# Kernel optimization log

Hardware: AMD Instinct MI355X
Metric: run time of the kernel (lower is better)

Reference implementation:

```python
import jax, jax.numpy as jnp
import numpy as np

# Model config (matches init_kwargs)
B, I, H, C = 2048, 1024, 2048, 1000   # batch, input_dim, hidden_dim, num_classes
S = 8                                  # num_wavefunctions
TOPK = 256
PARTIAL_NORM = 1.0
SM_STEPS = 2                           # self_modulation_steps
EPS = 1e-8


def setup_inputs() -> dict:
    key = jax.random.key(0)
    ks = jax.random.split(key, 9)
    x      = jax.random.normal(ks[0], (B, I), jnp.float32)
    # stacked per-wavefunction Linear(input_dim, 2*hidden_dim)
    W      = jax.random.normal(ks[1], (S, 2 * H, I), jnp.float32) * (1.0 / np.sqrt(I))
    b      = jax.random.normal(ks[2], (S, 2 * H), jnp.float32) * 0.01
    phases = jax.random.normal(ks[3], (S, H), jnp.float32) * 0.1   # phase_per_dim=True
    gate_W = jax.random.normal(ks[4], (H, H), jnp.float32) * (1.0 / np.sqrt(H))
    gate_b = jax.random.normal(ks[5], (H,), jnp.float32) * 0.01
    clf_W  = jax.random.normal(ks[6], (C, H), jnp.float32) * (1.0 / np.sqrt(H))
    clf_b  = jax.random.normal(ks[7], (C,), jnp.float32) * 0.01
    return {"x": x, "W": W, "b": b, "phases": phases,
            "gate_W": gate_W, "gate_b": gate_b, "clf_W": clf_W, "clf_b": clf_b}


def reference(x, W, b, phases, gate_W, gate_b, clf_W, clf_b):
    # All wavefunction branches batched into one GEMM: [B,S,2H]
    out = jnp.einsum('bi,shi->bsh', x, W) + b[None]
    out = jnp.exp(-(out * out))                      # ArcBell activation
    alpha, beta = out[..., :H], out[..., H:]         # [B,S,H] each
    norm_sq = jnp.sum(alpha * alpha + beta * beta, axis=-1, keepdims=True) + EPS
    factor = jnp.sqrt((PARTIAL_NORM * PARTIAL_NORM) / norm_sq)  # [B,S,1]
    alpha = alpha * factor
    beta = beta * factor
    cphi = jnp.cos(phases)[None]                     # [1,S,H]
    sphi = jnp.sin(phases)[None]
    # phase rotation + complex accumulate over wavefunctions
    sup_real = jnp.sum(alpha * cphi - beta * sphi, axis=1)   # [B,H]
    sup_imag = jnp.sum(alpha * sphi + beta * cphi, axis=1)
    # self-modulation (fixed small step count -> Python loop is fine)
    for _ in range(SM_STEPS):
        mag = jnp.sqrt(sup_real * sup_real + sup_imag * sup_imag)
        gate = jax.nn.sigmoid(mag @ gate_W.T + gate_b)
        sup_real = sup_real * gate
        sup_imag = sup_imag * gate
    mag_sq = sup_real * sup_real + sup_imag * sup_imag       # [B,H]
    # top-k masked probability aggregation
    _, idx = jax.lax.top_k(mag_sq, TOPK)                     # idx: [B,TOPK]
    mask = jnp.zeros_like(mag_sq).at[jnp.arange(B)[:, None], idx].set(1.0)
    masked = mag_sq * mask
    probs = masked / (jnp.sum(masked, axis=-1, keepdims=True) + EPS)
    logits = probs @ clf_W.T + clf_b                         # [B,C]
    return logits
```

## Files before the change

### kernel.cpp

```cpp
#include <hip/hip_runtime.h>

typedef _Float16 f16;
typedef _Float16 f16x8 __attribute__((ext_vector_type(8)));
typedef _Float16 f16x4 __attribute__((ext_vector_type(4)));
typedef float f32x4 __attribute__((ext_vector_type(4)));

#define B_    2048
#define I_    1024
#define H_    2048
#define C_    1000
#define S_    8
#define N1    32768
#define TOPK_ 256

__device__ __forceinline__ void gload16(const void* g, void* l) {
  __builtin_amdgcn_global_load_lds((const __attribute__((address_space(1))) void*)g,
                                   (__attribute__((address_space(3))) void*)l,
                                   16, 0, 0);
}

#define NW8  (S_ * 2 * H_ * I_ / 8)
#define NX8  (B_ * I_ / 8)
#define NG8  (H_ * H_ / 8)
#define NC8  (1024 * H_ / 8)
#define NPH  (S_ * H_)
#define NTOT (NW8 + NX8 + NG8 + NC8 + NPH)

__global__ void prep_kernel(const float* __restrict__ W, const float* __restrict__ x,
                            const float* __restrict__ gW, const float* __restrict__ cW,
                            const float* __restrict__ ph,
                            f16* __restrict__ Wf, f16* __restrict__ xf,
                            f16* __restrict__ gWf, f16* __restrict__ cWf,
                            float* __restrict__ cphi, float* __restrict__ sphi)
{
  int i = blockIdx.x * blockDim.x + threadIdx.x;
  if (i >= NTOT) return;
  if (i < NW8 + NX8 + NG8 + NC8) {
    const float* src;
    f16* dst;
    int j = i;
    bool pad = false;
    if (j < NW8)                { src = W;  dst = Wf; }
    else if ((j -= NW8) < NX8)  { src = x;  dst = xf; }
    else if ((j -= NX8) < NG8)  { src = gW; dst = gWf; }
    else {
      j -= NG8; src = cW; dst = cWf;
      pad = (j >= C_ * H_ / 8);
    }
    f16x8 o;
    if (!pad) {
      const float4 a = reinterpret_cast<const float4*>(src)[2 * j];
      const float4 b = reinterpret_cast<const float4*>(src)[2 * j + 1];
      o = (f16x8){ (f16)a.x, (f16)a.y, (f16)a.z, (f16)a.w,
                   (f16)b.x, (f16)b.y, (f16)b.z, (f16)b.w };
    } else {
      o = (f16x8){ (f16)0.f, (f16)0.f, (f16)0.f, (f16)0.f,
                   (f16)0.f, (f16)0.f, (f16)0.f, (f16)0.f };
    }
    reinterpret_cast<f16x8*>(dst)[j] = o;
  } else {
    int j = i - (NW8 + NX8 + NG8 + NC8);
    float p = ph[j];
    cphi[j] = cosf(p);
    sphi[j] = sinf(p);
  }
}

__global__ __launch_bounds__(512, 1)
void gemm1_r4(const f16* __restrict__ A, const f16* __restrict__ Bm,
              const float* __restrict__ bias, f16* __restrict__ act)
{
  __shared__ char SL[131072];
  const int tid = threadIdx.x, lane = tid & 63, wid = tid >> 6;
  const int wr = wid >> 2, wc = wid & 3;
  const int fr = lane & 15, fq = lane >> 4;
  const int bid = blockIdx.x;
  const int swz = (bid & 7) * 128 + (bid >> 3);
  const int mt = swz & 7, nt = swz >> 3;
  const long brow = (long)mt * 256, bcol = (long)nt * 256;

  const int schunk = ((tid & 3) ^ ((tid >> 3) & 3)) * 8;
  const f16* srcP[4];
  srcP[0] = A  + (brow + (tid >> 2)) * (long)I_ + schunk;
  srcP[1] = A  + (brow + 128 + (tid >> 2)) * (long)I_ + schunk;
  srcP[2] = Bm + (bcol + (tid >> 2)) * (long)I_ + schunk;
  srcP[3] = Bm + (bcol + 128 + (tid >> 2)) * (long)I_ + schunk;

  const int co = (fq ^ ((fr >> 1) & 3)) * 16;
  const int rdA0 = (wr * 128 + fr) * 64 + co;
  const int rdB0 = 16384 + (wc * 64 + fr) * 64 + co;

  f32x4 acc[8][4] = {};

#define STG1(a, tt)                                                    \
  gload16(srcP[a] + (size_t)(tt) * 32,                                 \
          SL + ((tt) & 3) * 32768 + ((a) * 512 + tid) * 16)

  STG1(0,0); STG1(1,0); STG1(2,0); STG1(3,0);
  STG1(0,1); STG1(1,1); STG1(2,1); STG1(3,1);
  STG1(0,2); STG1(1,2); STG1(2,2); STG1(3,2);
  asm volatile("s_waitcnt vmcnt(8)" ::: "memory");
  __builtin_amdgcn_s_barrier();

#pragma unroll 1
  for (int t = 0; t < 32; ++t) {
    const char* rb = SL + (t & 3) * 32768;
    if (t < 29) { STG1(0, t + 3); STG1(1, t + 3); STG1(2, t + 3); STG1(3, t + 3); }

    f16x8 bf[4], af[8];
#pragma unroll
    for (int n = 0; n < 4; ++n) bf[n] = *(const f16x8*)(rb + rdB0 + n * 1024);
#pragma unroll
    for (int i = 0; i < 8; ++i) af[i] = *(const f16x8*)(rb + rdA0 + i * 1024);

    __builtin_amdgcn_s_setprio(1);
#pragma unroll
    for (int i = 0; i < 8; ++i)
#pragma unroll
      for (int n = 0; n < 4; ++n)
        acc[i][n] = __builtin_amdgcn_mfma_f32_16x16x32_f16(af[i], bf[n], acc[i][n], 0, 0, 0);
    __builtin_amdgcn_s_setprio(0);

    if (t < 29)       asm volatile("s_waitcnt vmcnt(8)" ::: "memory");
    else if (t == 29) asm volatile("s_waitcnt vmcnt(4)" ::: "memory");
    else              asm volatile("s_waitcnt vmcnt(0)" ::: "memory");
    __builtin_amdgcn_s_barrier();
  }
#undef STG1

  float bv[4];
#pragma unroll
  for (int n = 0; n < 4; ++n) bv[n] = bias[bcol + wc * 64 + n * 16 + fr];
#pragma unroll
  for (int m = 0; m < 8; ++m) {
    const long r0 = brow + wr * 128 + m * 16 + fq * 4;
#pragma unroll
    for (int n = 0; n < 4; ++n) {
      const long c = bcol + wc * 64 + n * 16 + fr;
#pragma unroll
      for (int j = 0; j < 4; ++j) {
        const float tt = acc[m][n][j] + bv[n];
        act[(r0 + j) * (long)N1 + c] = (f16)__expf(-tt * tt);
      }
    }
  }
}

template<int BM, int BN, int WM, int WN, int THREADS, int MINW, int EPI>
__global__ __launch_bounds__(THREADS, MINW)
void gemm_ring(const f16* __restrict__ A, const f16* __restrict__ Bmat,
               const int K, const int MT, const int ldc, const int nreal,
               const float* __restrict__ bias,
               const float* __restrict__ magin,
               float* __restrict__ mago32, f16* __restrict__ mago16,
               float* __restrict__ msqout, float* __restrict__ logits)
{
  constexpr int MREP  = BM / (WM * 16);
  constexpr int NREP  = BN / (WN * 16);
  constexpr int CA    = (BM * 64) / (THREADS * 16);
  constexpr int CB    = (BN * 64) / (THREADS * 16);
  constexpr int CALLS = CA + CB;
  constexpr int SLOT  = (BM + BN) * 32;
  __shared__ f16 SL[4 * SLOT];

  const int tid  = threadIdx.x;
  const int lane = tid & 63, wid = tid >> 6;
  const int wr = wid / WN, wc = wid % WN;
  const int fr = lane & 15, fq = lane >> 4;

  const int nwg = gridDim.x;
  const int chunk = nwg >> 3;
  const int swz = (blockIdx.x & 7) * chunk + (blockIdx.x >> 3);
  const int mt = swz % MT, nt = swz / MT;
  const long brow = (long)mt * BM, bcol = (long)nt * BN;

  const f16* srcA[CA];
  const f16* srcB[CB];
#pragma unroll
  for (int a = 0; a < CA; ++a) {
    const int r = (a * THREADS + tid) >> 2;
    const int cs = (tid & 3) ^ ((r >> 1) & 3);
    srcA[a] = A + (size_t)(brow + r) * K + cs * 8;
  }
#pragma unroll
  for (int a = 0; a < CB; ++a) {
    const int r = (a * THREADS + tid) >> 2;
    const int cs = (tid & 3) ^ ((r >> 1) & 3);
    srcB[a] = Bmat + (size_t)(bcol + r) * K + cs * 8;
  }

  int ard[MREP], brd[NREP];
#pragma unroll
  for (int m = 0; m < MREP; ++m) {
    const int r = wr * MREP * 16 + m * 16 + fr;
    ard[m] = r * 32 + ((fq ^ ((r >> 1) & 3)) * 8);
  }
#pragma unroll
  for (int n = 0; n < NREP; ++n) {
    const int r = wc * NREP * 16 + n * 16 + fr;
    brd[n] = r * 32 + ((fq ^ ((r >> 1) & 3)) * 8);
  }

  f32x4 acc[MREP][NREP] = {};
  const int ntile = K >> 5;

#define STAGE_TILE(tt)                                                         \
  do {                                                                         \
    f16* D = &SL[((tt) & 3) * SLOT];                                           \
    const long kt = (long)(tt) * 32;                                           \
    _Pragma("unroll")                                                          \
    for (int a = 0; a < CA; ++a)                                               \
      gload16(srcA[a] + kt, D + a * THREADS * 8 + wid * 512);                  \
    _Pragma("unroll")                                                          \
    for (int a = 0; a < CB; ++a)                                               \
      gload16(srcB[a] + kt, D + BM * 32 + a * THREADS * 8 + wid * 512);        \
  } while (0)

  STAGE_TILE(0); STAGE_TILE(1); STAGE_TILE(2);

  for (int t = 0; t < ntile; ++t) {
    if (t + 3 < ntile) STAGE_TILE(t + 3);
    if (t < ntile - 3)       asm volatile("s_waitcnt vmcnt(%0)" :: "i"(3 * CALLS) : "memory");
    else if (t == ntile - 3) asm volatile("s_waitcnt vmcnt(%0)" :: "i"(2 * CALLS) : "memory");
    else if (t == ntile - 2) asm volatile("s_waitcnt vmcnt(%0)" :: "i"(1 * CALLS) : "memory");
    else                     asm volatile("s_waitcnt vmcnt(0)" ::: "memory");
    __builtin_amdgcn_s_barrier();
    asm volatile("" ::: "memory");

    const f16* SA = &SL[(t & 3) * SLOT];
    const f16* SB = SA + BM * 32;
    f16x8 af[MREP], bf[NREP];
#pragma unroll
    for (int m = 0; m < MREP; ++m) af[m] = *(const f16x8*)(SA + ard[m]);
#pragma unroll
    for (int n = 0; n < NREP; ++n) bf[n] = *(const f16x8*)(SB + brd[n]);

    __builtin_amdgcn_s_setprio(1);
#pragma unroll
    for (int m = 0; m < MREP; ++m)
#pragma unroll
      for (int n = 0; n < NREP; ++n)
        acc[m][n] = __builtin_amdgcn_mfma_f32_16x16x32_f16(af[m], bf[n], acc[m][n], 0, 0, 0);
    __builtin_amdgcn_s_setprio(0);
    asm volatile("" ::: "memory");
    __builtin_amdgcn_s_barrier();
  }
#undef STAGE_TILE

#pragma unroll
  for (int m = 0; m < MREP; ++m) {
    const long r0 = brow + wr * MREP * 16 + m * 16 + fq * 4;
#pragma unroll
    for (int n = 0; n < NREP; ++n) {
      const long c = bcol + wc * NREP * 16 + n * 16 + fr;
      float bv;
      if (EPI == 2) bv = (c < nreal) ? bias[c] : 0.f;
      else          bv = bias[c];
#pragma unroll
      for (int j = 0; j < 4; ++j) {
        const long r = r0 + j;
        const float t = acc[m][n][j] + bv;
        if (EPI == 1) {
          const float g = 1.f / (1.f + __expf(-t));
          const long idx = r * (long)ldc + c;
          const float v = magin[idx] * g;
          if (msqout) msqout[idx] = v * v;
          else { mago32[idx] = v; mago16[idx] = (f16)v; }
        } else {
          if (c < nreal) logits[r * (long)nreal + c] = t;
        }
      }
    }
  }
}

__global__ __launch_bounds__(512)
void normsup_kernel(const f16* __restrict__ act,
                    const float* __restrict__ cphi, const float* __restrict__ sphi,
                    float* __restrict__ mag32, f16* __restrict__ mag16)
{
  __shared__ float buf[4096];
  __shared__ float red[8];
  const int b = blockIdx.x, tid = threadIdx.x;
  const int lane = tid & 63, wv = tid >> 6;
  float sr[4] = {0, 0, 0, 0}, si[4] = {0, 0, 0, 0};
  const f16* base = act + (size_t)b * N1;

  for (int s = 0; s < S_; ++s) {
    f16x8 v = *(const f16x8*)(base + s * 4096 + tid * 8);
    float ls = 0.f;
#pragma unroll
    for (int e = 0; e < 8; ++e) {
      float f = (float)v[e];
      buf[tid * 8 + e] = f;
      ls += f * f;
    }
#pragma unroll
    for (int o = 32; o > 0; o >>= 1) ls += __shfl_down(ls, o);
    if (lane == 0) red[wv] = ls;
    __syncthreads();
    const float tot = red[0] + red[1] + red[2] + red[3] + red[4] + red[5] + red[6] + red[7];
    const float factor = 1.f / sqrtf(tot + 1e-8f);

    const float4 c4 = *(const float4*)(cphi + s * H_ + tid * 4);
    const float4 s4 = *(const float4*)(sphi + s * H_ + tid * 4);
    const float4 a4 = *(const float4*)(&buf[tid * 4]);
    const float4 b4 = *(const float4*)(&buf[2048 + tid * 4]);
    sr[0] += factor * (a4.x * c4.x - b4.x * s4.x); si[0] += factor * (a4.x * s4.x + b4.x * c4.x);
    sr[1] += factor * (a4.y * c4.y - b4.y * s4.y); si[1] += factor * (a4.y * s4.y + b4.y * c4.y);
    sr[2] += factor * (a4.z * c4.z - b4.z * s4.z); si[2] += factor * (a4.z * s4.z + b4.z * c4.z);
    sr[3] += factor * (a4.w * c4.w - b4.w * s4.w); si[3] += factor * (a4.w * s4.w + b4.w * c4.w);
    __syncthreads();
  }

  const size_t o = (size_t)b * H_ + tid * 4;
  const float m0 = sqrtf(sr[0] * sr[0] + si[0] * si[0]);
  const float m1 = sqrtf(sr[1] * sr[1] + si[1] * si[1]);
  const float m2 = sqrtf(sr[2] * sr[2] + si[2] * si[2]);
  const float m3 = sqrtf(sr[3] * sr[3] + si[3] * si[3]);
  *(float4*)(mag32 + o) = make_float4(m0, m1, m2, m3);
  f16x4 mh = { (f16)m0, (f16)m1, (f16)m2, (f16)m3 };
  *(f16x4*)(mag16 + o) = mh;
}

__global__ __launch_bounds__(256)
void topk_kernel(const float* __restrict__ msq, f16* __restrict__ probs)
{
  __shared__ unsigned vals[2048];
  __shared__ int hist[256];
  __shared__ int scn[256];
  __shared__ int sdig, sknew;
  __shared__ float wsum[4];
  const int b = blockIdx.x, tid = threadIdx.x;
  const unsigned* row = (const unsigned*)(msq + (size_t)b * H_);

  uint4 v0 = *(const uint4*)(row + tid * 8);
  uint4 v1 = *(const uint4*)(row + tid * 8 + 4);
  vals[tid * 8 + 0] = v0.x; vals[tid * 8 + 1] = v0.y;
  vals[tid * 8 + 2] = v0.z; vals[tid * 8 + 3] = v0.w;
  vals[tid * 8 + 4] = v1.x; vals[tid * 8 + 5] = v1.y;
  vals[tid * 8 + 6] = v1.z; vals[tid * 8 + 7] = v1.w;
  __syncthreads();

  int k = TOPK_;
  unsigned prefix = 0, pmask = 0;
  for (int pass = 0; pass < 4; ++pass) {
    const int sh = 24 - pass * 8;
    hist[tid] = 0;
    __syncthreads();
#pragma unroll
    for (int e = 0; e < 8; ++e) {
      unsigned v = vals[tid * 8 + e];
      if ((v & pmask) == prefix) atomicAdd(&hist[(v >> sh) & 255u], 1);
    }
    __syncthreads();
    const int own = hist[tid];
    int sc = own;
    scn[tid] = sc;
    __syncthreads();
    for (int o2 = 1; o2 < 256; o2 <<= 1) {
      int add = (tid + o2 < 256) ? scn[tid + o2] : 0;
      __syncthreads();
      sc += add; scn[tid] = sc;
      __syncthreads();
    }
    if (sc >= k && (sc - own) < k) { sdig = tid; sknew = k - (sc - own); }
    __syncthreads();
    prefix |= ((unsigned)sdig) << sh;
    pmask  |= 0xFFu << sh;
    k = sknew;
    __syncthreads();
  }

  const unsigned T = prefix;
  const int krem = k;
  unsigned vl[8];
  int eqc = 0;
#pragma unroll
  for (int e = 0; e < 8; ++e) { vl[e] = vals[tid * 8 + e]; if (vl[e] == T) eqc++; }
  int sc2 = eqc;
  scn[tid] = sc2;
  __syncthreads();
  for (int o2 = 1; o2 < 256; o2 <<= 1) {
    int add = (tid >= o2) ? scn[tid - o2] : 0;
    __syncthreads();
    sc2 += add; scn[tid] = sc2;
    __syncthreads();
  }
  int rank = sc2 - eqc;
  float ls = 0.f;
  bool sel[8];
#pragma unroll
  for (int e = 0; e < 8; ++e) {
    const unsigned v = vl[e];
    bool s_ = false;
    if (v > T) s_ = true;
    else if (v == T) { s_ = (rank < krem); ++rank; }
    sel[e] = s_;
    if (s_) ls += __uint_as_float(v);
  }
#pragma unroll
  for (int o2 = 32; o2 > 0; o2 >>= 1) ls += __shfl_down(ls, o2);
  if ((tid & 63) == 0) wsum[tid >> 6] = ls;
  __syncthreads();
  const float tot = wsum[0] + wsum[1] + wsum[2] + wsum[3];
  const float inv = 1.f / (tot + 1e-8f);
  f16x8 ov;
#pragma unroll
  for (int e = 0; e < 8; ++e)
    ov[e] = sel[e] ? (f16)(__uint_as_float(vl[e]) * inv) : (f16)0.f;
  *(f16x8*)(probs + (size_t)b * H_ + tid * 8) = ov;
}

extern "C" void kernel_launch(void* const* d_in, const int* in_sizes, int n_in,
                              void* d_out, int out_size, void* d_ws, size_t ws_size,
                              hipStream_t stream)
{
  const float* x  = (const float*)d_in[0];
  const float* W  = (const float*)d_in[1];
  const float* bb = (const float*)d_in[2];
  const float* ph = (const float*)d_in[3];
  const float* gW = (const float*)d_in[4];
  const float* gb = (const float*)d_in[5];
  const float* cW = (const float*)d_in[6];
  const float* cb = (const float*)d_in[7];
  float* out = (float*)d_out;

  char* base = (char*)d_ws;
  size_t off = 0;
  auto take = [&](size_t bytes) -> char* {
    char* r = base + off;
    off += (bytes + 255) & ~(size_t)255;
    return r;
  };
  f16*   Wf    = (f16*)  take((size_t)S_ * 2 * H_ * I_ * 2);
  f16*   xf    = (f16*)  take((size_t)B_ * I_ * 2);
  f16*   gWf   = (f16*)  take((size_t)H_ * H_ * 2);
  f16*   cWf   = (f16*)  take((size_t)1024 * H_ * 2);
  float* cphi  = (float*)take((size_t)S_ * H_ * 4);
  float* sphi  = (float*)take((size_t)S_ * H_ * 4);
  f16*   act   = (f16*)  take((size_t)B_ * N1 * 2);
  float* mag0f = (float*)take((size_t)B_ * H_ * 4);
  f16*   mag0h = (f16*)  take((size_t)B_ * H_ * 2);
  float* mag1f = (float*)take((size_t)B_ * H_ * 4);
  f16*   mag1h = (f16*)  take((size_t)B_ * H_ * 2);
  float* msq   = (float*)take((size_t)B_ * H_ * 4);
  f16*   probs = (f16*)  take((size_t)B_ * H_ * 2);
  (void)ws_size; (void)in_sizes; (void)n_in; (void)out_size;

  prep_kernel<<<(NTOT + 255) / 256, 256, 0, stream>>>(
      W, x, gW, cW, ph, Wf, xf, gWf, cWf, cphi, sphi);

  gemm1_r4<<<(B_ / 256) * (N1 / 256), 512, 0, stream>>>(xf, Wf, bb, act);

  normsup_kernel<<<B_, 512, 0, stream>>>(act, cphi, sphi, mag0f, mag0h);

  gemm_ring<128, 128, 2, 2, 256, 2, 1><<<(B_ / 128) * (H_ / 128), 256, 0, stream>>>(
      mag0h, gWf, H_, B_ / 128, H_, H_, gb,
      mag0f, mag1f, mag1h, nullptr, nullptr);

  gemm_ring<128, 128, 2, 2, 256, 2, 1><<<(B_ / 128) * (H_ / 128), 256, 0, stream>>>(
      mag1h, gWf, H_, B_ / 128, H_, H_, gb,
      mag1f, nullptr, nullptr, msq, nullptr);

  topk_kernel<<<B_, 256, 0, stream>>>(msq, probs);

  gemm_ring<128, 64, 2, 2, 256, 3, 2><<<(B_ / 128) * (1024 / 64), 256, 0, stream>>>(
      probs, cWf, H_, B_ / 128, 0, C_, cb,
      nullptr, nullptr, nullptr, nullptr, out);
}
```

Before: 374.5 us.

## Convert fp32 W to fp16 inside GEMM1 and retile gate GEMMs

Result: slower. 430.4 us (+14.9%).

```diff
diff --git a/kernel.cpp b/kernel.cpp
--- a/kernel.cpp
+++ b/kernel.cpp
@@ -19,29 +19,27 @@
                                    16, 0, 0);
 }
 
-#define NW8  (S_ * 2 * H_ * I_ / 8)
 #define NX8  (B_ * I_ / 8)
 #define NG8  (H_ * H_ / 8)
 #define NC8  (1024 * H_ / 8)
 #define NPH  (S_ * H_)
-#define NTOT (NW8 + NX8 + NG8 + NC8 + NPH)
-
-__global__ void prep_kernel(const float* __restrict__ W, const float* __restrict__ x,
+#define NTOT (NX8 + NG8 + NC8 + NPH)
+
+__global__ void prep_kernel(const float* __restrict__ x,
                             const float* __restrict__ gW, const float* __restrict__ cW,
                             const float* __restrict__ ph,
-                            f16* __restrict__ Wf, f16* __restrict__ xf,
+                            f16* __restrict__ xf,
                             f16* __restrict__ gWf, f16* __restrict__ cWf,
                             float* __restrict__ cphi, float* __restrict__ sphi)
 {
   int i = blockIdx.x * blockDim.x + threadIdx.x;
   if (i >= NTOT) return;
-  if (i < NW8 + NX8 + NG8 + NC8) {
+  if (i < NX8 + NG8 + NC8) {
     const float* src;
     f16* dst;
     int j = i;
     bool pad = false;
-    if (j < NW8)                { src = W;  dst = Wf; }
-    else if ((j -= NW8) < NX8)  { src = x;  dst = xf; }
+    if (j < NX8)                { src = x;  dst = xf; }
     else if ((j -= NX8) < NG8)  { src = gW; dst = gWf; }
     else {
       j -= NG8; src = cW; dst = cWf;
@@ -59,7 +57,7 @@
     }
     reinterpret_cast<f16x8*>(dst)[j] = o;
   } else {
-    int j = i - (NW8 + NX8 + NG8 + NC8);
+    int j = i - (NX8 + NG8 + NC8);
     float p = ph[j];
     cphi[j] = cosf(p);
     sphi[j] = sinf(p);
@@ -67,10 +65,10 @@
 }
 
 __global__ __launch_bounds__(512, 1)
-void gemm1_r4(const f16* __restrict__ A, const f16* __restrict__ Bm,
-              const float* __restrict__ bias, f16* __restrict__ act)
-{
-  __shared__ char SL[131072];
+void gemm1_w32(const f16* __restrict__ A, const float* __restrict__ BW,
+               const float* __restrict__ bias, f16* __restrict__ act)
+{
+  __shared__ char SL[98304];
   const int tid = threadIdx.x, lane = tid & 63, wid = tid >> 6;
   const int wr = wid >> 2, wc = wid & 3;
   const int fr = lane & 15, fq = lane >> 4;
@@ -80,38 +78,62 @@
   const long brow = (long)mt * 256, bcol = (long)nt * 256;
 
   const int schunk = ((tid & 3) ^ ((tid >> 3) & 3)) * 8;
-  const f16* srcP[4];
-  srcP[0] = A  + (brow + (tid >> 2)) * (long)I_ + schunk;
-  srcP[1] = A  + (brow + 128 + (tid >> 2)) * (long)I_ + schunk;
-  srcP[2] = Bm + (bcol + (tid >> 2)) * (long)I_ + schunk;
-  srcP[3] = Bm + (bcol + 128 + (tid >> 2)) * (long)I_ + schunk;
+  const f16* srcA0 = A + (brow + (tid >> 2)) * (long)I_ + schunk;
+  const f16* srcA1 = A + (brow + 128 + (tid >> 2)) * (long)I_ + schunk;
+
+  const int rB   = tid >> 1;
+  const int aSel = (tid & 1) ^ ((tid >> 3) & 1);
+  const int beta = (tid >> 2) & 1;
+  const float* bsrc = BW + (size_t)(bcol + rB) * I_ + aSel * 16;
+  char* wbase = SL + 65536 + tid * 32;
 
   const int co = (fq ^ ((fr >> 1) & 3)) * 16;
   const int rdA0 = (wr * 128 + fr) * 64 + co;
-  const int rdB0 = 16384 + (wc * 64 + fr) * 64 + co;
+  const int rdB0 = (wc * 64 + fr) * 64 + co;
 
   f32x4 acc[8][4] = {};
 
-#define STG1(a, tt)                                                    \
-  gload16(srcP[a] + (size_t)(tt) * 32,                                 \
-          SL + ((tt) & 3) * 32768 + ((a) * 512 + tid) * 16)
-
-  STG1(0,0); STG1(1,0); STG1(2,0); STG1(3,0);
-  STG1(0,1); STG1(1,1); STG1(2,1); STG1(3,1);
-  STG1(0,2); STG1(1,2); STG1(2,2); STG1(3,2);
-  asm volatile("s_waitcnt vmcnt(8)" ::: "memory");
-  __builtin_amdgcn_s_barrier();
+#define STGA(a, tt)                                                     \
+  gload16(((a) ? srcA1 : srcA0) + (size_t)(tt) * 32,                    \
+          SL + ((tt) & 3) * 16384 + ((a) * 512 + tid) * 16)
+#define LOADB(tt, v0, v1, v2, v3)                                       \
+  do { const float4* bp = (const float4*)(bsrc + (size_t)(tt) * 32);    \
+       v0 = bp[0]; v1 = bp[1]; v2 = bp[2]; v3 = bp[3]; } while (0)
+#define WRITEB(slot, v0, v1, v2, v3)                                    \
+  do { f16x8 h0 = { (f16)v0.x, (f16)v0.y, (f16)v0.z, (f16)v0.w,         \
+                    (f16)v1.x, (f16)v1.y, (f16)v1.z, (f16)v1.w };       \
+       f16x8 h1 = { (f16)v2.x, (f16)v2.y, (f16)v2.z, (f16)v2.w,         \
+                    (f16)v3.x, (f16)v3.y, (f16)v3.z, (f16)v3.w };       \
+       char* wb = wbase + (slot) * 16384;                               \
+       *(f16x8*)(wb + beta * 16) = h0;                                  \
+       *(f16x8*)(wb + (beta ^ 1) * 16) = h1; } while (0)
+
+  {
+    float4 p0, p1, p2, p3;
+    LOADB(0, p0, p1, p2, p3);
+    asm volatile("" ::: "memory");
+    STGA(0,0); STGA(1,0); STGA(0,1); STGA(1,1); STGA(0,2); STGA(1,2);
+    asm volatile("s_waitcnt vmcnt(4)" ::: "memory");
+    WRITEB(0, p0, p1, p2, p3);
+    asm volatile("s_waitcnt lgkmcnt(0)" ::: "memory");
+    __builtin_amdgcn_s_barrier();
+  }
 
 #pragma unroll 1
   for (int t = 0; t < 32; ++t) {
-    const char* rb = SL + (t & 3) * 32768;
-    if (t < 29) { STG1(0, t + 3); STG1(1, t + 3); STG1(2, t + 3); STG1(3, t + 3); }
-
+    float4 b0, b1, b2, b3;
+    if (t < 31) LOADB(t + 1, b0, b1, b2, b3);
+    asm volatile("" ::: "memory");
+    if (t < 29) { STGA(0, t + 3); STGA(1, t + 3); }
+    asm volatile("" ::: "memory");
+
+    const char* ra = SL + (t & 3) * 16384;
+    const char* rbB = SL + 65536 + (t & 1) * 16384;
     f16x8 bf[4], af[8];
 #pragma unroll
-    for (int n = 0; n < 4; ++n) bf[n] = *(const f16x8*)(rb + rdB0 + n * 1024);
-#pragma unroll
-    for (int i = 0; i < 8; ++i) af[i] = *(const f16x8*)(rb + rdA0 + i * 1024);
+    for (int n = 0; n < 4; ++n) bf[n] = *(const f16x8*)(rbB + rdB0 + n * 1024);
+#pragma unroll
+    for (int i = 0; i < 8; ++i) af[i] = *(const f16x8*)(ra + rdA0 + i * 1024);
 
     __builtin_amdgcn_s_setprio(1);
 #pragma unroll
@@ -121,12 +143,15 @@
         acc[i][n] = __builtin_amdgcn_mfma_f32_16x16x32_f16(af[i], bf[n], acc[i][n], 0, 0, 0);
     __builtin_amdgcn_s_setprio(0);
 
-    if (t < 29)       asm volatile("s_waitcnt vmcnt(8)" ::: "memory");
-    else if (t == 29) asm volatile("s_waitcnt vmcnt(4)" ::: "memory");
-    else              asm volatile("s_waitcnt vmcnt(0)" ::: "memory");
+    if (t < 29) asm volatile("s_waitcnt vmcnt(2)" ::: "memory");
+    else        asm volatile("s_waitcnt vmcnt(0)" ::: "memory");
+    if (t < 31) WRITEB((t + 1) & 1, b0, b1, b2, b3);
+    asm volatile("s_waitcnt lgkmcnt(0)" ::: "memory");
     __builtin_amdgcn_s_barrier();
   }
-#undef STG1
+#undef STGA
+#undef LOADB
+#undef WRITEB
 
   float bv[4];
 #pragma unroll
@@ -433,7 +458,6 @@
     off += (bytes + 255) & ~(size_t)255;
     return r;
   };
-  f16*   Wf    = (f16*)  take((size_t)S_ * 2 * H_ * I_ * 2);
   f16*   xf    = (f16*)  take((size_t)B_ * I_ * 2);
   f16*   gWf   = (f16*)  take((size_t)H_ * H_ * 2);
   f16*   cWf   = (f16*)  take((size_t)1024 * H_ * 2);
@@ -449,17 +473,17 @@
   (void)ws_size; (void)in_sizes; (void)n_in; (void)out_size;
 
   prep_kernel<<<(NTOT + 255) / 256, 256, 0, stream>>>(
-      W, x, gW, cW, ph, Wf, xf, gWf, cWf, cphi, sphi);
-
-  gemm1_r4<<<(B_ / 256) * (N1 / 256), 512, 0, stream>>>(xf, Wf, bb, act);
+      x, gW, cW, ph, xf, gWf, cWf, cphi, sphi);
+
+  gemm1_w32<<<(B_ / 256) * (N1 / 256), 512, 0, stream>>>(xf, W, bb, act);
 
   normsup_kernel<<<B_, 512, 0, stream>>>(act, cphi, sphi, mag0f, mag0h);
 
-  gemm_ring<128, 128, 2, 2, 256, 2, 1><<<(B_ / 128) * (H_ / 128), 256, 0, stream>>>(
+  gemm_ring<128, 64, 2, 2, 256, 3, 1><<<(B_ / 128) * (H_ / 64), 256, 0, stream>>>(
       mag0h, gWf, H_, B_ / 128, H_, H_, gb,
       mag0f, mag1f, mag1h, nullptr, nullptr);
 
-  gemm_ring<128, 128, 2, 2, 256, 2, 1><<<(B_ / 128) * (H_ / 128), 256, 0, stream>>>(
+  gemm_ring<128, 64, 2, 2, 256, 3, 1><<<(B_ / 128) * (H_ / 64), 256, 0, stream>>>(
       mag1h, gWf, H_, B_ / 128, H_, H_, gb,
       mag1f, nullptr, nullptr, msq, nullptr);
 
```
